# Kernel optimization log

Hardware: AMD Instinct MI355X
Metric: run time of the kernel (lower is better)

Reference implementation:

```python
import math
import jax, jax.numpy as jnp
import numpy as np

B, H, N, D = 1, 16, 4096, 64
SINK_SIZE = 32
NUM_PROJS = 7
BLOCK_SIZE = 256
SAMPLE_SIZE = 256
MIN_SEQ_LEN = 1024
_SAMPLE_KEY = jax.random.key(1234)

def _hamming_perm(num_projs):
    a = np.array([0, 1])
    for _ in range(num_projs - 1):
        a = np.concatenate([a, a[::-1] + a.shape[0]])
    return jnp.asarray(a, dtype=jnp.int32)

_PERM = _hamming_perm(NUM_PROJS)
_MASK = jnp.asarray(2 ** np.arange(NUM_PROJS), dtype=jnp.int32)

def lsh_hash(x, proj_dir):
    # x: [b,h,n,d], proj_dir: [d,r] -> Gray-code-permuted bucket ids [b,h,n]
    rotated = jnp.einsum('bhnd,dr->bhnr', x, proj_dir)
    bin_ids = jnp.sum((rotated > 0).astype(jnp.int32) * _MASK, axis=-1)
    return _PERM[bin_ids]

def indexing(x, idx, chunk_size=-1):
    # gather rows along axis 2, optionally zero-pad to a multiple of chunk_size
    out = jnp.take_along_axis(x, idx[..., None], axis=2)
    if chunk_size > 0 and out.shape[2] % chunk_size != 0:
        pad = (-out.shape[2]) % chunk_size
        out = jnp.pad(out, ((0, 0), (0, 0), (0, pad), (0, 0)))
    return out

def exact_attention(q, k, v, scale, causal=False, bias=None):
    qk = jnp.einsum('bhqd,bhkd->bhqk', q, k) * scale
    if causal:
        nq, nk = q.shape[2], k.shape[2]
        cmask = jnp.triu(jnp.full((nq, nk), jnp.finfo(q.dtype).min, dtype=q.dtype), k=1)
        qk = qk + cmask
    if bias is not None:
        qk = qk + bias
    lse = jax.nn.logsumexp(qk, axis=-1, keepdims=True)
    attn = jnp.einsum('bhqk,bhkd->bhqd', jnp.exp(qk - lse), v)
    return attn, lse

def add_self_attentions(attn1, lse1, attn2, lse2):
    # attn = (attn1*e^lse1 + attn2*e^lse2)/(e^lse1+e^lse2); lse = log(e^lse1+e^lse2)
    c = jax.nn.sigmoid(lse1 - lse2)
    attn = c * attn1 + (1 - c) * attn2
    lse = jnp.logaddexp(lse1, lse2)
    return attn, lse

def forward_no_causal_mask(q, k, v, scale, proj_dir, ctr):
    b, h, nq, d = q.shape
    nk = k.shape[2]
    if MIN_SEQ_LEN > nq:
        return exact_attention(q, k, v, scale, causal=False)
    # 1) sortLSH block-diagonal attention
    q_sort_idx = jnp.argsort(lsh_hash(q, proj_dir), axis=2)  # stable
    k_sort_idx = jnp.argsort(lsh_hash(k, proj_dir), axis=2)
    q_sort_idx_inv = jnp.argsort(q_sort_idx, axis=2)
    q_sorted = indexing(q, q_sort_idx, BLOCK_SIZE)
    k_sorted = indexing(k, k_sort_idx, BLOCK_SIZE)
    v_sorted = indexing(v, k_sort_idx, BLOCK_SIZE)
    num_blocks = k_sorted.shape[2] // BLOCK_SIZE
    q_block = q_sorted.shape[2] // num_blocks
    qs = q_sorted.reshape(-1, 1, q_block, d)
    ks = k_sorted.reshape(-1, 1, BLOCK_SIZE, d)
    vs = v_sorted.reshape(-1, 1, BLOCK_SIZE, d)
    attn_block, lse_block = exact_attention(qs, ks, vs, scale, causal=False)
    attn_block = attn_block.reshape(b, h, q_sorted.shape[2], d)[:, :, :nq, :]
    lse_block = lse_block.reshape(b, h, q_sorted.shape[2], 1)[:, :, :nq, :]
    q_sorted = q_sorted[:, :, :nq, :]
    k_sorted = k_sorted[:, :, :nk, :]
    v_sorted = v_sorted[:, :, :nk, :]
    # 2) residual via uniform sampling (block-diag entries masked out)
    if SAMPLE_SIZE > 0 and nq > q_block and nk > BLOCK_SIZE:
        skey = jax.random.fold_in(_SAMPLE_KEY, ctr[0]); ctr[0] += 1
        sampled = jax.random.randint(skey, (b, h, SAMPLE_SIZE), 0, nk)
        v_sub = indexing(v_sorted, sampled)
        k_sub = indexing(k_sorted, sampled)
        q_blk_id = jnp.arange(nq) // q_block                 # [nq]
        k_blk_id = sampled // BLOCK_SIZE                     # [b,h,s]
        bias = (q_blk_id[None, None, :, None] == k_blk_id[:, :, None, :]).astype(q.dtype) * jnp.finfo(q.dtype).min
        attn_res, lse_res = exact_attention(q_sorted, k_sub, v_sub, scale, causal=False, bias=bias)
        lse_res = lse_res + math.log(nk / SAMPLE_SIZE)
        attn, lse = add_self_attentions(attn_block, lse_block, attn_res, lse_res)
    else:
        attn, lse = attn_block, lse_block
    # restore original row order
    attn = indexing(attn, q_sort_idx_inv)
    lse = indexing(lse, q_sort_idx_inv)
    return attn, lse

def hyper_causal(q, k, v, scale, proj_dir, ctr):
    b, h, n, d = q.shape
    if n <= MIN_SEQ_LEN:
        return exact_attention(q, k, v, scale, causal=True)
    n_orig = n
    if n % 2:
        q = jnp.pad(q, ((0, 0), (0, 0), (0, 1), (0, 0)))
        k = jnp.pad(k, ((0, 0), (0, 0), (0, 1), (0, 0)))
        v = jnp.pad(v, ((0, 0), (0, 0), (0, 1), (0, 0)))
    half = q.shape[2] // 2
    # recurse on the two diagonal halves (folded into head dim)
    attn_bd, lse_bd = hyper_causal(q.reshape(b, 2 * h, half, d), k.reshape(b, 2 * h, half, d), v.reshape(b, 2 * h, half, d), scale, proj_dir, ctr)
    attn_bd = attn_bd.reshape(b, h, -1, d)
    lse_bd = lse_bd.reshape(b, h, -1, 1)
    # off-diagonal lower-left block, unmasked
    attn_un, lse_un = forward_no_causal_mask(q[:, :, half:, :], k[:, :, :half, :], v[:, :, :half, :], scale, proj_dir, ctr)
    attn_up, lse_up = attn_bd[:, :, :half, :], lse_bd[:, :, :half, :]
    attn_dn, lse_dn = add_self_attentions(attn_bd[:, :, half:, :], lse_bd[:, :, half:, :], attn_un, lse_un)
    attn = jnp.concatenate([attn_up, attn_dn], axis=2)
    lse = jnp.concatenate([lse_up, lse_dn], axis=2)
    if n_orig % 2:
        attn = attn[:, :, :-1, :]
        lse = lse[:, :, :-1, :]
    return attn, lse

def _forward(query, key, value, proj_dir):
    b, h, n, d = query.shape
    scale = d ** (-0.5)
    sink = min(SINK_SIZE, n)
    prefix_attn, prefix_lse = exact_attention(query, key[:, :, :sink, :], value[:, :, :sink, :], scale, causal=True)
    if sink >= n:
        return prefix_attn
    ctr = [0]
    tail_attn, tail_lse = hyper_causal(query[:, :, sink:, :], key[:, :, sink:, :], value[:, :, sink:, :], scale, proj_dir, ctr)
    padded_tail_attn = jnp.zeros_like(prefix_attn).at[:, :, sink:, :].set(tail_attn)
    neg_inf = jnp.full_like(prefix_lse[:, :, :sink, :], jnp.finfo(prefix_lse.dtype).min)
    padded_tail_lse = jnp.concatenate([neg_inf, tail_lse], axis=2)
    attn, _ = add_self_attentions(prefix_attn, prefix_lse, padded_tail_attn, padded_tail_lse)
    return attn

def setup_inputs() -> dict:
    rng = jax.random.key(0)
    k1, k2, k3, k4 = jax.random.split(rng, 4)
    return {
        'query': jax.random.normal(k1, (B, H, N, D), jnp.float32),
        'key': jax.random.normal(k2, (B, H, N, D), jnp.float32),
        'value': jax.random.normal(k3, (B, H, N, D), jnp.float32),
        'proj_dir': jax.random.normal(k4, (D, NUM_PROJS), jnp.float32),
    }

def reference(query, key, value, proj_dir):
    return _forward(query, key, value, proj_dir)
```

## Files before the change

### kernel.cpp

```cpp
#include <hip/hip_runtime.h>
#include <hip/hip_bf16.h>
#include <math.h>
#include <stdint.h>

#define H_ 16
#define N_ 4096
#define NT_ 4064
#define NL_ 2032
#define SINK_ 32
#define SAMP_ 256
#define SCALE_ 0.125f
#define QSCALE_ 0.18033688f
#define M0L2_ 11.5415606f
#define M0_ 8.0f
#define NEGBIG_ -3.0e38f
#define LOGOFF_L2_ 2.9886841f

typedef unsigned int uint;
typedef unsigned short ushort;
typedef short bf16x8 __attribute__((ext_vector_type(8)));
typedef float f32x4 __attribute__((ext_vector_type(4)));

union B8 { uint4 u; bf16x8 b; };

__device__ __forceinline__ f32x4 mfma16(const B8& a, const B8& b, f32x4 c) {
  return __builtin_amdgcn_mfma_f32_16x16x32_bf16(a.b, b.b, c, 0, 0, 0);
}

__device__ __forceinline__ uint bfpack(float a, float b) {
  uint ua = __float_as_uint(a), ub = __float_as_uint(b);
  ua += 0x7fffu + ((ua >> 16) & 1u);
  ub += 0x7fffu + ((ub >> 16) & 1u);
  return (ua >> 16) | (ub & 0xffff0000u);
}

__device__ __forceinline__ uint cvtpk(float a, float b) {
  union { __hip_bfloat162 h; uint u; } r;
  r.h.x = __float2bfloat16(a);
  r.h.y = __float2bfloat16(b);
  return r.u;
}

__device__ __forceinline__ float logaddexpf_(float a, float b) {
  float mx = fmaxf(a, b);
  return mx + __logf(__expf(a - mx) + __expf(b - mx));
}

__device__ __forceinline__ uint32_t rotl32_(uint32_t v, uint32_t d) {
  return (v << d) | (v >> (32u - d));
}

__device__ inline void tf2x32(uint32_t k0, uint32_t k1, uint32_t& x0, uint32_t& x1) {
  uint32_t ks2 = k0 ^ k1 ^ 0x1BD11BDAu;
  x0 += k0; x1 += k1;
#define TFR(r) { x0 += x1; x1 = rotl32_(x1, r); x1 ^= x0; }
  TFR(13u) TFR(15u) TFR(26u) TFR(6u)
  x0 += k1;  x1 += ks2 + 1u;
  TFR(17u) TFR(29u) TFR(16u) TFR(24u)
  x0 += ks2; x1 += k0 + 2u;
  TFR(13u) TFR(15u) TFR(26u) TFR(6u)
  x0 += k0;  x1 += k1 + 3u;
  TFR(17u) TFR(29u) TFR(16u) TFR(24u)
  x0 += k1;  x1 += ks2 + 4u;
  TFR(13u) TFR(15u) TFR(26u) TFR(6u)
  x0 += ks2; x1 += k0 + 5u;
#undef TFR
}

__device__ __forceinline__ void nomax_sm(f32x4 s[4], float& ssum) {
#pragma unroll
  for (int st = 0; st < 4; ++st)
#pragma unroll
    for (int r = 0; r < 4; ++r) {
      s[st][r] = __builtin_exp2f(s[st][r]);
      ssum += s[st][r];
    }
}

__device__ __forceinline__ void pv144(const f32x4 s[4], f32x4 o[4],
                                      const char* vbase, char* pw, int g) {
  __builtin_amdgcn_s_setprio(1);
#pragma unroll
  for (int hk2 = 0; hk2 < 2; ++hk2) {
    const f32x4 pa = s[2 * hk2], pc = s[2 * hk2 + 1];
    *(uint2*)(pw + 8 * g)      = make_uint2(cvtpk(pa[0], pa[1]), cvtpk(pa[2], pa[3]));
    *(uint2*)(pw + 32 + 8 * g) = make_uint2(cvtpk(pc[0], pc[1]), cvtpk(pc[2], pc[3]));
    B8 pf, vf;
    pf.u = *(const uint4*)(pw + g * 16);
    vf.u = *(const uint4*)(vbase + 0 * 2304 + hk2 * 64); o[0] = mfma16(vf, pf, o[0]);
    vf.u = *(const uint4*)(vbase + 1 * 2304 + hk2 * 64); o[1] = mfma16(vf, pf, o[1]);
    vf.u = *(const uint4*)(vbase + 2 * 2304 + hk2 * 64); o[2] = mfma16(vf, pf, o[2]);
    vf.u = *(const uint4*)(vbase + 3 * 2304 + hk2 * 64); o[3] = mfma16(vf, pf, o[3]);
  }
  __builtin_amdgcn_s_setprio(0);
}

__global__ __launch_bounds__(256) void kern_packhash(
    const float* __restrict__ K, const float* __restrict__ V, const float* __restrict__ Q,
    const float* __restrict__ proj,
    ushort* __restrict__ Kb, ushort* __restrict__ Vb, ushort* __restrict__ Vt,
    int* __restrict__ hq, int* __restrict__ hk) {
  const int bb = blockIdx.x;
  const int tid = threadIdx.x;
  if (bb < 2048) {
    const size_t idx = (size_t)bb * 256 + tid;
    const float4* s = (const float4*)(K + idx * 8);
    float4 f0 = s[0], f1 = s[1];
    uint4 p = make_uint4(bfpack(f0.x, f0.y), bfpack(f0.z, f0.w),
                         bfpack(f1.x, f1.y), bfpack(f1.z, f1.w));
    *(uint4*)(Kb + idx * 8) = p;
    return;
  }
  if (bb < 3072) {
    __shared__ ushort tr[64 * 72];
    const int u = bb - 2048;
    const int h = u >> 6, nt = u & 63;
    const int n0 = nt * 64;
    const size_t hN = (size_t)h * N_;
    const int nloc = tid >> 2, dpart = (tid & 3) * 16;
    const float4* src = (const float4*)(V + (hN + n0 + nloc) * 64 + dpart);
    float4 f0 = src[0], f1 = src[1], f2 = src[2], f3 = src[3];
    uint p0 = bfpack(f0.x, f0.y), p1 = bfpack(f0.z, f0.w);
    uint p2 = bfpack(f1.x, f1.y), p3 = bfpack(f1.z, f1.w);
    uint p4 = bfpack(f2.x, f2.y), p5 = bfpack(f2.z, f2.w);
    uint p6 = bfpack(f3.x, f3.y), p7 = bfpack(f3.z, f3.w);
    ushort* vbdst = Vb + (hN + n0 + nloc) * 64 + dpart;
    ((uint4*)vbdst)[0] = make_uint4(p0, p1, p2, p3);
    ((uint4*)vbdst)[1] = make_uint4(p4, p5, p6, p7);
    uint pv[8] = {p0, p1, p2, p3, p4, p5, p6, p7};
#pragma unroll
    for (int j = 0; j < 8; ++j) {
      tr[(dpart + 2 * j    ) * 72 + nloc] = (ushort)(pv[j] & 0xffffu);
      tr[(dpart + 2 * j + 1) * 72 + nloc] = (ushort)(pv[j] >> 16);
    }
    __syncthreads();
    const int d = tid >> 2, np = (tid & 3) * 16;
    const uint4* tp = (const uint4*)(tr + d * 72 + np);
    uint4 t0 = tp[0], t1 = tp[1];
    ushort* dst = Vt + ((size_t)(h * 64 + d)) * 4096 + n0 + np;
    ((uint4*)dst)[0] = t0;
    ((uint4*)dst)[1] = t1;
    return;
  }
  __shared__ float pr[448];
  const int u = bb - 3072;
  const int h = u & 15, tile = (u >> 4) & 7, which = u >> 7;
  for (int t = tid; t < 448; t += 256) pr[t] = proj[t];
  __syncthreads();
  const int i = tile * 256 + tid;
  if (i >= NL_) return;
  const int orig = (which == 0) ? (SINK_ + NL_ + i) : (SINK_ + i);
  const float4* x = (const float4*)((which == 0 ? Q : K) + ((size_t)h * N_ + orig) * 64);
  float xr[64];
#pragma unroll
  for (int d = 0; d < 16; ++d) {
    float4 g = x[d];
    xr[4*d+0] = g.x; xr[4*d+1] = g.y; xr[4*d+2] = g.z; xr[4*d+3] = g.w;
  }
  int bin = 0;
#pragma unroll
  for (int r = 0; r < 7; ++r) {
    float acc = 0.f;
#pragma unroll
    for (int d = 0; d < 64; ++d) acc = fmaf(xr[d], pr[d * 7 + r], acc);
    if (acc > 0.f) bin |= (1 << r);
  }
  const int g = bin ^ (bin >> 1);
  (which == 0 ? hq : hk)[h * NL_ + i] = g;
}

__global__ __launch_bounds__(256) void kern_sortsamp(
    const int* __restrict__ hq, const int* __restrict__ hk,
    int* __restrict__ q_sort, int* __restrict__ k_sort,
    int* __restrict__ samp_pos, int* __restrict__ samp_orig) {
  const int h = blockIdx.x, which = blockIdx.y;
  const int tid = threadIdx.x;

  __shared__ unsigned char keys8[NL_];
  __shared__ ushort M[64 * 130];
  __shared__ int btot[128];
  __shared__ int bscan[128];
  __shared__ ushort srt[NL_];

  const int* src = (which == 0 ? hq : hk) + h * NL_;
  for (int u = tid; u < 64 * 130 / 2; u += 256) ((uint*)M)[u] = 0u;
  for (int u = tid; u < NL_; u += 256) keys8[u] = (unsigned char)src[u];
  __syncthreads();

  if (tid < 64) {
    const int c = tid;
#pragma unroll 4
    for (int j = 0; j < 32; ++j) {
      const int u = c * 32 + j;
      if (u < NL_) ++M[c * 130 + keys8[u]];
    }
  }
  __syncthreads();

  if (tid < 128) {
    const int b = tid;
    int run = 0;
    for (int c = 0; c < 64; ++c) {
      const int v = M[c * 130 + b];
      M[c * 130 + b] = (ushort)run;
      run += v;
    }
    btot[b] = run;
    bscan[b] = run;
  }
  __syncthreads();

  for (int ofs = 1; ofs < 128; ofs <<= 1) {
    int v = 0;
    if (tid < 128 && tid >= ofs) v = bscan[tid - ofs];
    __syncthreads();
    if (tid < 128) bscan[tid] += v;
    __syncthreads();
  }

  int* dst = (which == 0 ? q_sort : k_sort) + h * NL_;
  if (tid < 64) {
    const int c = tid;
    for (int j = 0; j < 32; ++j) {
      const int u = c * 32 + j;
      if (u < NL_) {
        const int k = keys8[u];
        const int pos = (bscan[k] - btot[k]) + M[c * 130 + k];
        M[c * 130 + k] += 1;
        dst[pos] = u;
        srt[pos] = (ushort)u;
      }
    }
  }
  __syncthreads();

  if (which == 1) {
    const int s = tid;
    uint32_t a0 = 0u, a1 = 0u; tf2x32(0u, 1234u, a0, a1);
    uint32_t b0 = 0u, b1 = 0u; tf2x32(a0, a1, b0, b1);
    uint32_t c0 = 0u, c1 = 1u; tf2x32(a0, a1, c0, c1);
    const uint32_t j = (uint32_t)(h * SAMP_ + s);
    uint32_t h0 = 0u, h1 = j; tf2x32(b0, b1, h0, h1);
    uint32_t l0 = 0u, l1 = j; tf2x32(c0, c1, l0, l1);
    const uint32_t Hb = h0 ^ h1, Lb = l0 ^ l1;
    const uint32_t off = ((Hb % 2032u) * 16u + (Lb % 2032u)) % 2032u;
    samp_pos[h * SAMP_ + s] = (int)off;
    samp_orig[h * SAMP_ + s] = (int)srt[off];
  }
}

__global__ __launch_bounds__(256) void kern_attn_mfma(
    const float* __restrict__ Q, const ushort* __restrict__ Kb, const ushort* __restrict__ Vt,
    float* __restrict__ tail_attn, float* __restrict__ tail_lse,
    float* __restrict__ attn2, float* __restrict__ lse2) {
  __shared__ uint kk[4608];
  __shared__ uint vv[4352];
  __shared__ uint pbuf[1280];

  const int b = blockIdx.x;
  const int tid = threadIdx.x;
  const int lane = tid & 63, w = tid >> 6;
  const int g = lane >> 4, q = lane & 15;
  const uint4 z4 = make_uint4(0, 0, 0, 0);
  const f32x4 accb = {-M0L2_, -M0L2_, -M0L2_, -M0L2_};

  int h, q0, qbase, kbase, ntiles, klen, p2slot = 0, chunkc = 0;
  bool causal;
  if (b < 512) {
    const int u = b; const int vh = u & 63;
    const int qt = 7 - (u >> 6);
    h = vh >> 2; chunkc = vh & 3;
    q0 = qt * 128;
    qbase = SINK_ + chunkc * 1016;
    kbase = qbase;
    ntiles = qt + 1; causal = true; klen = 1016;
  } else {
    const int u = b - 512; const int vh = u & 31; const int qt = (u >> 5) & 7;
    const int hf = u >> 8;
    h = vh >> 1; const int pp = vh & 1;
    q0 = qt * 128;
    qbase = SINK_ + pp * 2032 + 1016;
    kbase = SINK_ + pp * 2032 + hf * 512;
    ntiles = 4; causal = false; klen = hf ? 504 : 512;
    p2slot = hf * 32 * 1016 + vh * 1016;
  }
  const size_t hN = (size_t)h * N_;
  const int qrowA = q0 + w * 16 + q;
  const int qrowB = qrowA + 64;
  const int qcA = min(qrowA, 1015), qcB = min(qrowB, 1015);
  const int qwA_lo = q0 + w * 16, qwmaxA = qwA_lo + 15;
  const int qwB_lo = qwA_lo + 64;

  B8 qbA0, qbA1, qbB0, qbB1;
  {
    const float4* qp = (const float4*)(Q + (hN + qbase + qcA) * 64);
    float4 a = qp[2*g], c = qp[2*g+1], d = qp[8+2*g], e = qp[8+2*g+1];
    qbA0.u = make_uint4(bfpack(a.x*QSCALE_, a.y*QSCALE_), bfpack(a.z*QSCALE_, a.w*QSCALE_),
                        bfpack(c.x*QSCALE_, c.y*QSCALE_), bfpack(c.z*QSCALE_, c.w*QSCALE_));
    qbA1.u = make_uint4(bfpack(d.x*QSCALE_, d.y*QSCALE_), bfpack(d.z*QSCALE_, d.w*QSCALE_),
                        bfpack(e.x*QSCALE_, e.y*QSCALE_), bfpack(e.z*QSCALE_, e.w*QSCALE_));
    const float4* qp2 = (const float4*)(Q + (hN + qbase + qcB) * 64);
    a = qp2[2*g]; c = qp2[2*g+1]; d = qp2[8+2*g]; e = qp2[8+2*g+1];
    qbB0.u = make_uint4(bfpack(a.x*QSCALE_, a.y*QSCALE_), bfpack(a.z*QSCALE_, a.w*QSCALE_),
                        bfpack(c.x*QSCALE_, c.y*QSCALE_), bfpack(c.z*QSCALE_, c.w*QSCALE_));
    qbB1.u = make_uint4(bfpack(d.x*QSCALE_, d.y*QSCALE_), bfpack(d.z*QSCALE_, d.w*QSCALE_),
                        bfpack(e.x*QSCALE_, e.y*QSCALE_), bfpack(e.z*QSCALE_, e.w*QSCALE_));
  }
  f32x4 oA[4] = {{0,0,0,0},{0,0,0,0},{0,0,0,0},{0,0,0,0}};
  f32x4 oB[4] = {{0,0,0,0},{0,0,0,0},{0,0,0,0},{0,0,0,0}};
  float ssA = 0.f, ssB = 0.f;

  const int krow_l = tid >> 1, kpart = tid & 1;
  const int vrow = tid >> 2, vc32 = tid & 3;
  char* kdst = (char*)kk + krow_l * 144 + kpart * 64;
  char* vdst = (char*)vv + vrow * 272 + vc32 * 64;
  const char* kq = (const char*)kk + q * 144 + g * 16;
  const char* vq = (const char*)vv + q * 272 + g * 16;
  char* pw = (char*)pbuf + w * 1280 + q * 80;
  const size_t vtbase = ((size_t)(h * 64 + vrow)) * 4096 + kbase + vc32 * 32;

  uint4 kp0, kp1, kp2, kp3, va, va2, vb_, vb2;

#define LOADK(T) { const int kr = (T) * 128 + krow_l; \
    if (kr < klen) { const uint4* s = (const uint4*)(Kb + (hN + kbase + kr) * 64 + kpart * 32); \
      kp0 = s[0]; kp1 = s[1]; kp2 = s[2]; kp3 = s[3]; } \
    else { kp0 = z4; kp1 = z4; kp2 = z4; kp3 = z4; } }
#define LOADV(T) { const uint4* sv = (const uint4*)(Vt + vtbase + (size_t)(T) * 128); \
    va = sv[0]; va2 = sv[1]; vb_ = sv[2]; vb2 = sv[3]; }

  LOADK(0) LOADV(0)

  for (int t = 0; t < ntiles; ++t) {
    const int kt = t * 128;
    __syncthreads();
    *(uint4*)kdst = kp0; *(uint4*)(kdst + 16) = kp1;
    *(uint4*)(kdst + 32) = kp2; *(uint4*)(kdst + 48) = kp3;
    *(uint4*)vdst = va; *(uint4*)(vdst + 16) = va2;
    *(uint4*)(vdst + 32) = vb_; *(uint4*)(vdst + 48) = vb2;
    __syncthreads();
    if (t + 1 < ntiles) { LOADK(t + 1) LOADV(t + 1) }

#pragma unroll
    for (int u2 = 0; u2 < 2; ++u2) {
      const int hb = kt + u2 * 64;
      const bool dA = !(causal && hb > qwmaxA);
      f32x4 sA[4], sB[4];
      __builtin_amdgcn_s_setprio(1);
#pragma unroll
      for (int st = 0; st < 4; ++st) {
        B8 ka, kb2;
        ka.u  = *(const uint4*)(kq + (u2 * 64 + st * 16) * 144);
        kb2.u = *(const uint4*)(kq + (u2 * 64 + st * 16) * 144 + 64);
        if (dA) {
          f32x4 acc = accb;
          acc = mfma16(ka, qbA0, acc); acc = mfma16(kb2, qbA1, acc);
          sA[st] = acc;
        }
        f32x4 acc2 = accb;
        acc2 = mfma16(ka, qbB0, acc2); acc2 = mfma16(kb2, qbB1, acc2);
        sB[st] = acc2;
      }
      __builtin_amdgcn_s_setprio(0);

      if (causal) {
        const int kb0 = hb + 4 * g;
        if (dA && hb + 63 > qwA_lo) {
#pragma unroll
          for (int st = 0; st < 4; ++st)
#pragma unroll
            for (int r = 0; r < 4; ++r)
              if (kb0 + st * 16 + r > qrowA) sA[st][r] = NEGBIG_;
        }
        if (hb + 63 > qwB_lo) {
#pragma unroll
          for (int st = 0; st < 4; ++st)
#pragma unroll
            for (int r = 0; r < 4; ++r)
              if (kb0 + st * 16 + r > qrowB) sB[st][r] = NEGBIG_;
        }
      } else if (hb + 63 >= klen) {
        const int kb0 = hb + 4 * g;
#pragma unroll
        for (int st = 0; st < 4; ++st)
#pragma unroll
          for (int r = 0; r < 4; ++r)
            if (kb0 + st * 16 + r >= klen) { sA[st][r] = NEGBIG_; sB[st][r] = NEGBIG_; }
      }

#define PVX(SS, OO) { \
      __builtin_amdgcn_s_setprio(1); \
      _Pragma("unroll") \
      for (int hk2 = 0; hk2 < 2; ++hk2) { \
        const f32x4 pa = SS[2 * hk2], pc = SS[2 * hk2 + 1]; \
        *(uint2*)(pw + 8 * g)      = make_uint2(cvtpk(pa[0], pa[1]), cvtpk(pa[2], pa[3])); \
        *(uint2*)(pw + 32 + 8 * g) = make_uint2(cvtpk(pc[0], pc[1]), cvtpk(pc[2], pc[3])); \
        B8 pf, vf; \
        pf.u = *(const uint4*)(pw + g * 16); \
        const int vo = u2 * 128 + hk2 * 64; \
        vf.u = *(const uint4*)(vq + 0 * 4352 + vo); OO[0] = mfma16(vf, pf, OO[0]); \
        vf.u = *(const uint4*)(vq + 1 * 4352 + vo); OO[1] = mfma16(vf, pf, OO[1]); \
        vf.u = *(const uint4*)(vq + 2 * 4352 + vo); OO[2] = mfma16(vf, pf, OO[2]); \
        vf.u = *(const uint4*)(vq + 3 * 4352 + vo); OO[3] = mfma16(vf, pf, OO[3]); \
      } \
      __builtin_amdgcn_s_setprio(0); }

      if (dA) {
        nomax_sm(sA, ssA);
        PVX(sA, oA)
      }
      nomax_sm(sB, ssB);
      PVX(sB, oB)
#undef PVX
    }
  }
#undef LOADK
#undef LOADV

  ssA += __shfl_xor(ssA, 16); ssA += __shfl_xor(ssA, 32);
  ssB += __shfl_xor(ssB, 16); ssB += __shfl_xor(ssB, 32);
#pragma unroll
  for (int fr = 0; fr < 2; ++fr) {
    const int qrow = fr == 0 ? qrowA : qrowB;
    if (qrow >= 1016) continue;
    f32x4* o = fr == 0 ? oA : oB;
    const float ss = fr == 0 ? ssA : ssB;
    const float lse = M0_ + __logf(ss);
    const float inv = 1.f / ss;
    if (causal) {
      const int trow = chunkc * 1016 + qrow;
      float* tp = tail_attn + ((size_t)h * NT_ + trow) * 64;
      *(f32x4*)(tp +  0 + 4*g) = o[0] * inv;
      *(f32x4*)(tp + 16 + 4*g) = o[1] * inv;
      *(f32x4*)(tp + 32 + 4*g) = o[2] * inv;
      *(f32x4*)(tp + 48 + 4*g) = o[3] * inv;
      if (lane < 16) tail_lse[h * NT_ + trow] = lse;
    } else {
      float* tp = attn2 + ((size_t)(p2slot + qrow)) * 64;
      *(f32x4*)(tp +  0 + 4*g) = o[0] * inv;
      *(f32x4*)(tp + 16 + 4*g) = o[1] * inv;
      *(f32x4*)(tp + 32 + 4*g) = o[2] * inv;
      *(f32x4*)(tp + 48 + 4*g) = o[3] * inv;
      if (lane < 16) lse2[p2slot + qrow] = lse;
    }
  }
}

__global__ __launch_bounds__(256) void kern_lsh_mfma(
    const float* __restrict__ Q, const ushort* __restrict__ Kb, const ushort* __restrict__ Vb,
    const int* __restrict__ q_sort, const int* __restrict__ k_sort,
    const int* __restrict__ samp_pos, const int* __restrict__ samp_orig,
    float* __restrict__ attn3, float* __restrict__ lse3) {
  __shared__ uint kk[2304];
  __shared__ uint vv[2304];
  __shared__ uint pbuf[1280];
  __shared__ float bias_s[64];

  const int b = blockIdx.x;
  const int which = b >> 8;
  const int bq = b & 255;
  const int h = bq >> 4, pt = bq & 15;
  const int tid = threadIdx.x;
  const int lane = tid & 63, w = tid >> 6;
  const int g = lane >> 4, q = lane & 15;
  const int blkq = pt >> 1;
  const size_t hN = (size_t)h * N_;

  const int pA = pt * 128 + w * 16 + q;
  const int pB = pA + 64;
  const int qiA = q_sort[h * NL_ + min(pA, NL_ - 1)];
  const int qiB = q_sort[h * NL_ + min(pB, NL_ - 1)];

  const int skey = tid >> 2, kpart = tid & 3;
  const int kpi = tid & 31, vdb = (tid >> 5) * 8;
  int kidx[4], vi0[4], vi1[4];
  float biasr[4];
#pragma unroll
  for (int t = 0; t < 4; ++t) {
    if (which == 0) {
      const int slot = blkq * 256 + t * 64 + skey;
      kidx[t] = (slot < NL_) ? k_sort[h * NL_ + slot] : -1;
      const int s0 = blkq * 256 + t * 64 + 2 * kpi;
      vi0[t] = (s0 < NL_) ? k_sort[h * NL_ + s0] : -1;
      vi1[t] = (s0 + 1 < NL_) ? k_sort[h * NL_ + s0 + 1] : -1;
    } else {
      kidx[t] = samp_orig[h * SAMP_ + t * 64 + skey];
      const int si = t * 64 + 2 * kpi;
      vi0[t] = samp_orig[h * SAMP_ + si];
      vi1[t] = samp_orig[h * SAMP_ + si + 1];
    }
  }
  if (which == 1 && tid < 64) {
#pragma unroll
    for (int j = 0; j < 4; ++j)
      biasr[j] = ((samp_pos[h * SAMP_ + j * 64 + tid] >> 8) == blkq) ? NEGBIG_ : LOGOFF_L2_;
  }

  B8 qbA0, qbA1, qbB0, qbB1;
  {
    const float4* qp = (const float4*)(Q + (hN + SINK_ + NL_ + qiA) * 64);
    float4 a = qp[2*g], c = qp[2*g+1], d = qp[8+2*g], e = qp[8+2*g+1];
    qbA0.u = make_uint4(bfpack(a.x*QSCALE_, a.y*QSCALE_), bfpack(a.z*QSCALE_, a.w*QSCALE_),
                        bfpack(c.x*QSCALE_, c.y*QSCALE_), bfpack(c.z*QSCALE_, c.w*QSCALE_));
    qbA1.u = make_uint4(bfpack(d.x*QSCALE_, d.y*QSCALE_), bfpack(d.z*QSCALE_, d.w*QSCALE_),
                        bfpack(e.x*QSCALE_, e.y*QSCALE_), bfpack(e.z*QSCALE_, e.w*QSCALE_));
    const float4* qp2 = (const float4*)(Q + (hN + SINK_ + NL_ + qiB) * 64);
    a = qp2[2*g]; c = qp2[2*g+1]; d = qp2[8+2*g]; e = qp2[8+2*g+1];
    qbB0.u = make_uint4(bfpack(a.x*QSCALE_, a.y*QSCALE_), bfpack(a.z*QSCALE_, a.w*QSCALE_),
                        bfpack(c.x*QSCALE_, c.y*QSCALE_), bfpack(c.z*QSCALE_, c.w*QSCALE_));
    qbB1.u = make_uint4(bfpack(d.x*QSCALE_, d.y*QSCALE_), bfpack(d.z*QSCALE_, d.w*QSCALE_),
                        bfpack(e.x*QSCALE_, e.y*QSCALE_), bfpack(e.z*QSCALE_, e.w*QSCALE_));
  }
  f32x4 oA[4] = {{0,0,0,0},{0,0,0,0},{0,0,0,0},{0,0,0,0}};
  f32x4 oB[4] = {{0,0,0,0},{0,0,0,0},{0,0,0,0},{0,0,0,0}};
  float ssA = 0.f, ssB = 0.f;
  const f32x4 accb = {-M0L2_, -M0L2_, -M0L2_, -M0L2_};

  char* kdst = (char*)kk + skey * 144 + kpart * 32;
  char* vdst = (char*)vv + vdb * 144 + kpi * 4;
  const char* kq = (const char*)kk + q * 144 + g * 16;
  const char* vq = (const char*)vv + q * 144 + g * 16;
  char* pw = (char*)pbuf + w * 1280 + q * 80;

  const uint4 z4 = make_uint4(0, 0, 0, 0);
  uint4 kp0, kp1, va, vb_;

#define LLOADK(T) { const int kr = kidx[T]; \
    if (kr >= 0) { const uint4* s = (const uint4*)(Kb + (hN + SINK_ + kr) * 64 + kpart * 16); \
      kp0 = s[0]; kp1 = s[1]; } else { kp0 = z4; kp1 = z4; } }
#define LLOADV(T) { const int r0 = vi0[T], r1 = vi1[T]; \
    va  = (r0 >= 0) ? *(const uint4*)(Vb + (hN + SINK_ + r0) * 64 + vdb) : z4; \
    vb_ = (r1 >= 0) ? *(const uint4*)(Vb + (hN + SINK_ + r1) * 64 + vdb) : z4; }

  LLOADK(0) LLOADV(0)

  for (int t = 0; t < 4; ++t) {
    __syncthreads();
    *(uint4*)kdst = kp0; *(uint4*)(kdst + 16) = kp1;
#define VP(JW, AW, BW) { \
    *(uint*)(vdst + (2*(JW)) * 144) = (AW & 0xffffu) | (BW << 16); \
    *(uint*)(vdst + (2*(JW) + 1) * 144) = (AW >> 16) | (BW & 0xffff0000u); }
    VP(0, va.x, vb_.x) VP(1, va.y, vb_.y) VP(2, va.z, vb_.z) VP(3, va.w, vb_.w)
#undef VP
    if (which == 1 && tid < 64) bias_s[tid] = biasr[t];
    __syncthreads();
    if (t + 1 < 4) { LLOADK(t + 1) LLOADV(t + 1) }

    f32x4 sA[4], sB[4];
    __builtin_amdgcn_s_setprio(1);
#pragma unroll
    for (int st = 0; st < 4; ++st) {
      B8 ka, kb2;
      ka.u  = *(const uint4*)(kq + (st * 16) * 144);
      kb2.u = *(const uint4*)(kq + (st * 16) * 144 + 64);
      f32x4 acc = accb;
      acc = mfma16(ka, qbA0, acc); acc = mfma16(kb2, qbA1, acc);
      sA[st] = acc;
      f32x4 acc2 = accb;
      acc2 = mfma16(ka, qbB0, acc2); acc2 = mfma16(kb2, qbB1, acc2);
      sB[st] = acc2;
    }
    __builtin_amdgcn_s_setprio(0);
    if (which == 1) {
      const f32x4* bp = (const f32x4*)bias_s;
#pragma unroll
      for (int st = 0; st < 4; ++st) {
        sA[st] = sA[st] + bp[st * 4 + g];
        sB[st] = sB[st] + bp[st * 4 + g];
      }
    }

    nomax_sm(sA, ssA);
    pv144(sA, oA, vq, pw, g);
    nomax_sm(sB, ssB);
    pv144(sB, oB, vq, pw, g);
  }
#undef LLOADK
#undef LLOADV

  ssA += __shfl_xor(ssA, 16); ssA += __shfl_xor(ssA, 32);
  ssB += __shfl_xor(ssB, 16); ssB += __shfl_xor(ssB, 32);
  const size_t obase = (size_t)which * 16 * NL_;
#pragma unroll
  for (int fr = 0; fr < 2; ++fr) {
    const int p = fr == 0 ? pA : pB;
    if (p >= NL_) continue;
    const int qi = fr == 0 ? qiA : qiB;
    f32x4* o = fr == 0 ? oA : oB;
    const float ss = fr == 0 ? ssA : ssB;
    const float un = M0_ + __logf(ss);
    const float inv = 1.f / ss;
    float* tp = attn3 + (obase + (size_t)h * NL_ + qi) * 64;
    *(f32x4*)(tp +  0 + 4*g) = o[0] * inv;
    *(f32x4*)(tp + 16 + 4*g) = o[1] * inv;
    *(f32x4*)(tp + 32 + 4*g) = o[2] * inv;
    *(f32x4*)(tp + 48 + 4*g) = o[3] * inv;
    if (lane < 16) lse3[obase + h * NL_ + qi] = un;
  }
}

__global__ __launch_bounds__(256) void kern_final(
    const float* __restrict__ Q, const float* __restrict__ K, const float* __restrict__ V,
    const float* __restrict__ tail_attn, const float* __restrict__ tail_lse,
    const float* __restrict__ attn2, const float* __restrict__ lse2,
    const float* __restrict__ attn3, const float* __restrict__ lse3,
    float* __restrict__ out) {
  const int h = blockIdx.x;
  const int r = blockIdx.y * 256 + (int)threadIdx.x;

  __shared__ float4 kk[SINK_ * 16];
  __shared__ float4 vv[SINK_ * 16];
  for (int u = threadIdx.x; u < SINK_ * 16; u += 256) {
    const int row = u >> 4, d4 = u & 15;
    kk[u] = ((const float4*)(K + ((size_t)h * N_ + row) * 64))[d4];
    vv[u] = ((const float4*)(V + ((size_t)h * N_ + row) * 64))[d4];
  }
  __syncthreads();

  float4 q4[16], acc[16];
  const float4* qp = (const float4*)(Q + ((size_t)h * N_ + r) * 64);
#pragma unroll
  for (int d = 0; d < 16; ++d) { q4[d] = qp[d]; acc[d] = make_float4(0.f, 0.f, 0.f, 0.f); }

  float ssum = 0.f;
  const int nk = min(SINK_, r + 1);
  for (int j = 0; j < nk; ++j) {
    float s = 0.f;
#pragma unroll
    for (int d = 0; d < 16; ++d) {
      float4 x = q4[d], y = kk[j * 16 + d];
      s = fmaf(x.x, y.x, s); s = fmaf(x.y, y.y, s);
      s = fmaf(x.z, y.z, s); s = fmaf(x.w, y.w, s);
    }
    const float wgt = __expf(fmaf(s, SCALE_, -M0_));
    ssum += wgt;
    const float4* v4 = &vv[j * 16];
#pragma unroll
    for (int d = 0; d < 16; ++d) {
      acc[d].x = fmaf(wgt, v4[d].x, acc[d].x);
      acc[d].y = fmaf(wgt, v4[d].y, acc[d].y);
      acc[d].z = fmaf(wgt, v4[d].z, acc[d].z);
      acc[d].w = fmaf(wgt, v4[d].w, acc[d].w);
    }
  }
  const float pl = M0_ + __logf(ssum);
  const float inv = 1.f / ssum;
  float4* op = (float4*)(out + ((size_t)h * N_ + r) * 64);
  if (r < SINK_) {
#pragma unroll
    for (int d = 0; d < 16; ++d)
      op[d] = make_float4(acc[d].x * inv, acc[d].y * inv, acc[d].z * inv, acc[d].w * inv);
    return;
  }

  const int t = r - SINK_;
  float4 a[16];
  const float4* tp = (const float4*)(tail_attn + ((size_t)h * NT_ + t) * 64);
#pragma unroll
  for (int d = 0; d < 16; ++d) a[d] = tp[d];
  float al = tail_lse[h * NT_ + t];

  const int pp = (t >= NL_) ? 1 : 0;
  const int tloc = t - pp * NL_;
  if (tloc >= 1016) {
    const int vh = h * 2 + pp, i = tloc - 1016;
    const float l20 = lse2[vh * 1016 + i];
    const float l21 = lse2[32 * 1016 + vh * 1016 + i];
    const float c12 = 1.f / (1.f + __expf(l21 - l20));
    const float l2 = logaddexpf_(l20, l21);
    const float c = 1.f / (1.f + __expf(l2 - al));
    const float4* b0 = (const float4*)(attn2 + ((size_t)(vh * 1016 + i)) * 64);
    const float4* b1 = (const float4*)(attn2 + ((size_t)(32 * 1016 + vh * 1016 + i)) * 64);
#pragma unroll
    for (int d = 0; d < 16; ++d) {
      const float4 x0 = b0[d], x1 = b1[d];
      const float4 bb = make_float4(c12 * x0.x + (1.f - c12) * x1.x,
                                    c12 * x0.y + (1.f - c12) * x1.y,
                                    c12 * x0.z + (1.f - c12) * x1.z,
                                    c12 * x0.w + (1.f - c12) * x1.w);
      a[d] = make_float4(c * a[d].x + (1.f - c) * bb.x,
                         c * a[d].y + (1.f - c) * bb.y,
                         c * a[d].z + (1.f - c) * bb.z,
                         c * a[d].w + (1.f - c) * bb.w);
    }
    al = logaddexpf_(al, l2);
  }
  if (t >= NL_) {
    const int qi = t - NL_;
    const float l3a = lse3[h * NL_ + qi];
    const float l3b = lse3[16 * NL_ + h * NL_ + qi];
    const float c34 = 1.f / (1.f + __expf(l3b - l3a));
    const float l3 = logaddexpf_(l3a, l3b);
    const float c = 1.f / (1.f + __expf(l3 - al));
    const float4* b0 = (const float4*)(attn3 + ((size_t)(h * NL_ + qi)) * 64);
    const float4* b1 = (const float4*)(attn3 + ((size_t)(16 * NL_ + h * NL_ + qi)) * 64);
#pragma unroll
    for (int d = 0; d < 16; ++d) {
      const float4 x0 = b0[d], x1 = b1[d];
      const float4 bb = make_float4(c34 * x0.x + (1.f - c34) * x1.x,
                                    c34 * x0.y + (1.f - c34) * x1.y,
                                    c34 * x0.z + (1.f - c34) * x1.z,
                                    c34 * x0.w + (1.f - c34) * x1.w);
      a[d] = make_float4(c * a[d].x + (1.f - c) * bb.x,
                         c * a[d].y + (1.f - c) * bb.y,
                         c * a[d].z + (1.f - c) * bb.z,
                         c * a[d].w + (1.f - c) * bb.w);
    }
    al = logaddexpf_(al, l3);
  }
  const float cc = 1.f / (1.f + __expf(al - pl));
#pragma unroll
  for (int d = 0; d < 16; ++d)
    op[d] = make_float4(cc * acc[d].x * inv + (1.f - cc) * a[d].x,
                        cc * acc[d].y * inv + (1.f - cc) * a[d].y,
                        cc * acc[d].z * inv + (1.f - cc) * a[d].z,
                        cc * acc[d].w * inv + (1.f - cc) * a[d].w);
}

extern "C" void kernel_launch(void* const* d_in, const int* in_sizes, int n_in,
                              void* d_out, int out_size, void* d_ws, size_t ws_size,
                              hipStream_t stream) {
  (void)in_sizes; (void)n_in; (void)out_size; (void)ws_size;
  const float* Q = (const float*)d_in[0];
  const float* K = (const float*)d_in[1];
  const float* V = (const float*)d_in[2];
  const float* proj = (const float*)d_in[3];
  float* out = (float*)d_out;

  char* w = (char*)d_ws;
  auto carve = [&](size_t bytes) { char* p = w; w += (bytes + 255) & ~(size_t)255; return p; };
  float* tail_attn = (float*)carve((size_t)H_ * NT_ * 64 * sizeof(float));
  float* tail_lse  = (float*)carve((size_t)H_ * NT_ * sizeof(float));
  float* attn2     = (float*)carve((size_t)2 * 32 * 1016 * 64 * sizeof(float));
  float* lse2      = (float*)carve((size_t)2 * 32 * 1016 * sizeof(float));
  float* attn3     = (float*)carve((size_t)2 * H_ * NL_ * 64 * sizeof(float));
  float* lse3      = (float*)carve((size_t)2 * H_ * NL_ * sizeof(float));
  ushort* Kb     = (ushort*)carve((size_t)H_ * N_ * 64 * sizeof(ushort));
  ushort* Vb     = (ushort*)carve((size_t)H_ * N_ * 64 * sizeof(ushort));
  ushort* Vt     = (ushort*)carve((size_t)H_ * N_ * 64 * sizeof(ushort) + 4096);
  int* hq        = (int*)carve((size_t)H_ * NL_ * sizeof(int));
  int* hk        = (int*)carve((size_t)H_ * NL_ * sizeof(int));
  int* q_sort    = (int*)carve((size_t)H_ * NL_ * sizeof(int));
  int* k_sort    = (int*)carve((size_t)H_ * NL_ * sizeof(int));
  int* samp_pos  = (int*)carve((size_t)H_ * SAMP_ * sizeof(int));
  int* samp_orig = (int*)carve((size_t)H_ * SAMP_ * sizeof(int));

  kern_packhash<<<dim3(3328), 256, 0, stream>>>(K, V, Q, proj, Kb, Vb, Vt, hq, hk);
  kern_sortsamp<<<dim3(H_, 2), 256, 0, stream>>>(hq, hk, q_sort, k_sort, samp_pos, samp_orig);
  kern_attn_mfma<<<dim3(1024), 256, 0, stream>>>(Q, Kb, Vt, tail_attn, tail_lse, attn2, lse2);
  kern_lsh_mfma<<<dim3(512), 256, 0, stream>>>(Q, Kb, Vb, q_sort, k_sort, samp_pos, samp_orig,
                                               attn3, lse3);
  kern_final<<<dim3(H_, 16), 256, 0, stream>>>(Q, K, V, tail_attn, tail_lse,
                                               attn2, lse2, attn3, lse3, out);
}
```

Measured before the change: 134.0 us.

## Split long causal diagonal blocks into two key halves merged via LSE

The causal attention blocks for the upper query tiles (4-7) are split into two work items. One covers the first 512 keys, unmasked. The other covers the remaining causal keys, with an offset mask. The partial results go to a new attn4/lse4 buffer and are merged in the final kernel with a sigmoid/logaddexp combine. This is meant to shorten the longest blocks (8 tiles down to at most 4) and balance the grid, at the cost of more blocks, an extra global round-trip of partial outputs, and extra work in the merge kernel.

```diff
diff --git a/kernel.cpp b/kernel.cpp
--- a/kernel.cpp
+++ b/kernel.cpp
@@ -252,7 +252,8 @@
 __global__ __launch_bounds__(256) void kern_attn_mfma(
     const float* __restrict__ Q, const ushort* __restrict__ Kb, const ushort* __restrict__ Vt,
     float* __restrict__ tail_attn, float* __restrict__ tail_lse,
-    float* __restrict__ attn2, float* __restrict__ lse2) {
+    float* __restrict__ attn2, float* __restrict__ lse2,
+    float* __restrict__ attn4, float* __restrict__ lse4) {
   __shared__ uint kk[4608];
   __shared__ uint vv[4352];
   __shared__ uint pbuf[1280];
@@ -264,18 +265,10 @@
   const uint4 z4 = make_uint4(0, 0, 0, 0);
   const f32x4 accb = {-M0L2_, -M0L2_, -M0L2_, -M0L2_};
 
-  int h, q0, qbase, kbase, ntiles, klen, p2slot = 0, chunkc = 0;
+  int h, q0, qbase, kbase, ntiles, klen, koff = 0, p2slot = 0, chunkc = 0, outmode;
   bool causal;
   if (b < 512) {
-    const int u = b; const int vh = u & 63;
-    const int qt = 7 - (u >> 6);
-    h = vh >> 2; chunkc = vh & 3;
-    q0 = qt * 128;
-    qbase = SINK_ + chunkc * 1016;
-    kbase = qbase;
-    ntiles = qt + 1; causal = true; klen = 1016;
-  } else {
-    const int u = b - 512; const int vh = u & 31; const int qt = (u >> 5) & 7;
+    const int u = b; const int vh = u & 31; const int qt = (u >> 5) & 7;
     const int hf = u >> 8;
     h = vh >> 1; const int pp = vh & 1;
     q0 = qt * 128;
@@ -283,12 +276,41 @@
     kbase = SINK_ + pp * 2032 + hf * 512;
     ntiles = 4; causal = false; klen = hf ? 504 : 512;
     p2slot = hf * 32 * 1016 + vh * 1016;
+    outmode = 1;
+  } else if (b < 768) {
+    const int u = b - 512; const int vh = u & 63;
+    const int qt = 4 + (u >> 6);
+    h = vh >> 2; chunkc = vh & 3;
+    q0 = qt * 128;
+    qbase = SINK_ + chunkc * 1016;
+    kbase = qbase;
+    ntiles = 4; causal = false; klen = 512;
+    outmode = 0;
+  } else if (b < 1024) {
+    const int u = b - 768; const int vh = u & 63;
+    const int qt = 7 - (u >> 6);
+    h = vh >> 2; chunkc = vh & 3;
+    q0 = qt * 128;
+    qbase = SINK_ + chunkc * 1016;
+    kbase = qbase + 512;
+    ntiles = qt - 3; causal = true; klen = 504; koff = 512;
+    outmode = 2;
+  } else {
+    const int u = b - 1024; const int vh = u & 63;
+    const int qt = 3 - (u >> 6);
+    h = vh >> 2; chunkc = vh & 3;
+    q0 = qt * 128;
+    qbase = SINK_ + chunkc * 1016;
+    kbase = qbase;
+    ntiles = qt + 1; causal = true; klen = 1016;
+    outmode = 0;
   }
   const size_t hN = (size_t)h * N_;
   const int qrowA = q0 + w * 16 + q;
   const int qrowB = qrowA + 64;
   const int qcA = min(qrowA, 1015), qcB = min(qrowB, 1015);
-  const int qwA_lo = q0 + w * 16, qwmaxA = qwA_lo + 15;
+  const int qeA = qrowA - koff, qeB = qrowB - koff;
+  const int qwA_lo = q0 + w * 16 - koff, qwmaxA = qwA_lo + 15;
   const int qwB_lo = qwA_lo + 64;
 
   B8 qbA0, qbA1, qbB0, qbB1;
@@ -369,14 +391,14 @@
           for (int st = 0; st < 4; ++st)
 #pragma unroll
             for (int r = 0; r < 4; ++r)
-              if (kb0 + st * 16 + r > qrowA) sA[st][r] = NEGBIG_;
+              if (kb0 + st * 16 + r > qeA) sA[st][r] = NEGBIG_;
         }
         if (hb + 63 > qwB_lo) {
 #pragma unroll
           for (int st = 0; st < 4; ++st)
 #pragma unroll
             for (int r = 0; r < 4; ++r)
-              if (kb0 + st * 16 + r > qrowB) sB[st][r] = NEGBIG_;
+              if (kb0 + st * 16 + r > qeB) sB[st][r] = NEGBIG_;
         }
       } else if (hb + 63 >= klen) {
         const int kb0 = hb + 4 * g;
@@ -426,22 +448,25 @@
     const float ss = fr == 0 ? ssA : ssB;
     const float lse = M0_ + __logf(ss);
     const float inv = 1.f / ss;
-    if (causal) {
+    float* tp;
+    float* lp;
+    if (outmode == 0) {
       const int trow = chunkc * 1016 + qrow;
-      float* tp = tail_attn + ((size_t)h * NT_ + trow) * 64;
-      *(f32x4*)(tp +  0 + 4*g) = o[0] * inv;
-      *(f32x4*)(tp + 16 + 4*g) = o[1] * inv;
-      *(f32x4*)(tp + 32 + 4*g) = o[2] * inv;
-      *(f32x4*)(tp + 48 + 4*g) = o[3] * inv;
-      if (lane < 16) tail_lse[h * NT_ + trow] = lse;
+      tp = tail_attn + ((size_t)h * NT_ + trow) * 64;
+      lp = tail_lse + h * NT_ + trow;
+    } else if (outmode == 1) {
+      tp = attn2 + ((size_t)(p2slot + qrow)) * 64;
+      lp = lse2 + p2slot + qrow;
     } else {
-      float* tp = attn2 + ((size_t)(p2slot + qrow)) * 64;
-      *(f32x4*)(tp +  0 + 4*g) = o[0] * inv;
-      *(f32x4*)(tp + 16 + 4*g) = o[1] * inv;
-      *(f32x4*)(tp + 32 + 4*g) = o[2] * inv;
-      *(f32x4*)(tp + 48 + 4*g) = o[3] * inv;
-      if (lane < 16) lse2[p2slot + qrow] = lse;
-    }
+      const int trow = chunkc * 1016 + qrow;
+      tp = attn4 + ((size_t)h * NT_ + trow) * 64;
+      lp = lse4 + h * NT_ + trow;
+    }
+    *(f32x4*)(tp +  0 + 4*g) = o[0] * inv;
+    *(f32x4*)(tp + 16 + 4*g) = o[1] * inv;
+    *(f32x4*)(tp + 32 + 4*g) = o[2] * inv;
+    *(f32x4*)(tp + 48 + 4*g) = o[3] * inv;
+    if (lane < 16) *lp = lse;
   }
 }
 
@@ -603,6 +628,7 @@
     const float* __restrict__ tail_attn, const float* __restrict__ tail_lse,
     const float* __restrict__ attn2, const float* __restrict__ lse2,
     const float* __restrict__ attn3, const float* __restrict__ lse3,
+    const float* __restrict__ attn4, const float* __restrict__ lse4,
     float* __restrict__ out) {
   const int h = blockIdx.x;
   const int r = blockIdx.y * 256 + (int)threadIdx.x;
@@ -658,6 +684,23 @@
 #pragma unroll
   for (int d = 0; d < 16; ++d) a[d] = tp[d];
   float al = tail_lse[h * NT_ + t];
+
+  const int chunk = t / 1016;
+  const int qrow = t - chunk * 1016;
+  if (qrow >= 512) {
+    const float l4 = lse4[h * NT_ + t];
+    const float c = 1.f / (1.f + __expf(l4 - al));
+    const float4* bp = (const float4*)(attn4 + ((size_t)h * NT_ + t) * 64);
+#pragma unroll
+    for (int d = 0; d < 16; ++d) {
+      const float4 bb = bp[d];
+      a[d] = make_float4(c * a[d].x + (1.f - c) * bb.x,
+                         c * a[d].y + (1.f - c) * bb.y,
+                         c * a[d].z + (1.f - c) * bb.z,
+                         c * a[d].w + (1.f - c) * bb.w);
+    }
+    al = logaddexpf_(al, l4);
+  }
 
   const int pp = (t >= NL_) ? 1 : 0;
   const int tloc = t - pp * NL_;
@@ -734,6 +777,8 @@
   float* lse2      = (float*)carve((size_t)2 * 32 * 1016 * sizeof(float));
   float* attn3     = (float*)carve((size_t)2 * H_ * NL_ * 64 * sizeof(float));
   float* lse3      = (float*)carve((size_t)2 * H_ * NL_ * sizeof(float));
+  float* attn4     = (float*)carve((size_t)H_ * NT_ * 64 * sizeof(float));
+  float* lse4      = (float*)carve((size_t)H_ * NT_ * sizeof(float));
   ushort* Kb     = (ushort*)carve((size_t)H_ * N_ * 64 * sizeof(ushort));
   ushort* Vb     = (ushort*)carve((size_t)H_ * N_ * 64 * sizeof(ushort));
   ushort* Vt     = (ushort*)carve((size_t)H_ * N_ * 64 * sizeof(ushort) + 4096);
@@ -746,9 +791,10 @@
 
   kern_packhash<<<dim3(3328), 256, 0, stream>>>(K, V, Q, proj, Kb, Vb, Vt, hq, hk);
   kern_sortsamp<<<dim3(H_, 2), 256, 0, stream>>>(hq, hk, q_sort, k_sort, samp_pos, samp_orig);
-  kern_attn_mfma<<<dim3(1024), 256, 0, stream>>>(Q, Kb, Vt, tail_attn, tail_lse, attn2, lse2);
+  kern_attn_mfma<<<dim3(1280), 256, 0, stream>>>(Q, Kb, Vt, tail_attn, tail_lse,
+                                                 attn2, lse2, attn4, lse4);
   kern_lsh_mfma<<<dim3(512), 256, 0, stream>>>(Q, Kb, Vb, q_sort, k_sort, samp_pos, samp_orig,
                                                attn3, lse3);
   kern_final<<<dim3(H_, 16), 256, 0, stream>>>(Q, K, V, tail_attn, tail_lse,
-                                               attn2, lse2, attn3, lse3, out);
-}
+                                               attn2, lse2, attn3, lse3, attn4, lse4, out);
+}
```

Measured after the change: 138.1 us. 3.1% more time.
